# Kernel optimization log

Measured on AMD Instinct MI355X. Metric: run time of the kernel, lower is better.

Reference implementation:

```python
import jax, jax.numpy as jnp
import numpy as np

DIM = 1024
HEADS = 16
HEAD_DIM = DIM // HEADS
SCALE = HEAD_DIM ** -0.5


def setup_inputs() -> dict:
    key = jax.random.key(0)
    k1, k2, k3, k4 = jax.random.split(key, 4)
    x = jax.random.normal(k1, (8, 1024, DIM), dtype=jnp.float32)
    # qkv: Linear(dim, 3*dim), bias=False; proj: Linear(dim, dim) with bias
    w_qkv = jax.random.normal(k2, (DIM, 3 * DIM), dtype=jnp.float32) * (DIM ** -0.5)
    w_proj = jax.random.normal(k3, (DIM, DIM), dtype=jnp.float32) * (DIM ** -0.5)
    b_proj = jax.random.normal(k4, (DIM,), dtype=jnp.float32) * 0.02
    return {"x": x, "w_qkv": w_qkv, "w_proj": w_proj, "b_proj": b_proj}


def reference(x, w_qkv, w_proj, b_proj):
    b, n, dim = x.shape
    h, d = HEADS, HEAD_DIM
    qkv = x @ w_qkv                                  # [b, n, 3*dim]
    qkv = qkv.reshape(b, n, 3, h, d)                  # split (qkv h d)
    q = jnp.transpose(qkv[:, :, 0], (0, 2, 1, 3))     # [b, h, n, d]
    k = jnp.transpose(qkv[:, :, 1], (0, 2, 1, 3))
    v = jnp.transpose(qkv[:, :, 2], (0, 2, 1, 3))
    dots = jnp.einsum('bhid,bhjd->bhij', q, k) * SCALE
    attn = jax.nn.softmax(dots, axis=-1)              # [b, h, n, n]
    out = jnp.einsum('bhij,bhjd->bhid', attn, v)      # [b, h, n, d]
    out = jnp.transpose(out, (0, 2, 1, 3)).reshape(b, n, dim)
    return out @ w_proj + b_proj
```

## Files before the change

### kernel.cpp

```cpp
#include <hip/hip_runtime.h>
#include <hip/hip_bf16.h>
#include <stdint.h>


typedef __attribute__((ext_vector_type(8))) short  short8;
typedef __attribute__((ext_vector_type(4))) float  floatx4;

#define MFMA_BF16(a, b, c) __builtin_amdgcn_mfma_f32_16x16x32_bf16((a), (b), (c), 0, 0, 0)

__device__ __forceinline__ uint16_t f2b(float f) {
    uint32_t i; __builtin_memcpy(&i, &f, 4);
    uint32_t r = i + 0x7FFFu + ((i >> 16) & 1u);
    return (uint16_t)(r >> 16);
}

__device__ __forceinline__ uint32_t pk_bf16(float a, float b) {
    uint32_t u;
    asm("v_cvt_pk_bf16_f32 %0, %1, %2" : "=v"(u) : "v"(a), "v"(b));
    return u;
}

__device__ __forceinline__ float exp2_hw(float x) {
    float r; asm("v_exp_f32 %0, %1" : "=v"(r) : "v"(x)); return r;
}

__device__ __forceinline__ void p32swap(uint32_t& a, uint32_t& b) {
    asm("v_permlane32_swap_b32 %0, %1" : "+v"(a), "+v"(b));
}
__device__ __forceinline__ void p16swap(uint32_t& a, uint32_t& b) {
    asm("v_permlane16_swap_b32 %0, %1" : "+v"(a), "+v"(b));
}

__device__ __forceinline__ void async16(uint16_t* lds, const uint16_t* g) {
    __builtin_amdgcn_global_load_lds(
        (const __attribute__((address_space(1))) uint32_t*)g,
        (__attribute__((address_space(3))) uint32_t*)lds,
        16, 0, 0);
}

__global__ __launch_bounds__(256) void cvt_f32_bf16(
    const float* __restrict__ in, uint16_t* __restrict__ out, int n4)
{
    const int i = blockIdx.x * 256 + threadIdx.x;
    if (i < n4) {
        const float4 v = ((const float4*)in)[i];
        ushort4 o;
        o.x = f2b(v.x); o.y = f2b(v.y); o.z = f2b(v.z); o.w = f2b(v.w);
        ((ushort4*)out)[i] = o;
    }
}

__global__ __launch_bounds__(256) void transpose_k(
    const float* __restrict__ in, uint16_t* __restrict__ out, int R, int C)
{
    __shared__ uint16_t t[32][33];
    const int bx = blockIdx.x * 32;
    const int by = blockIdx.y * 32;
    const int tx = threadIdx.x & 31, ty = threadIdx.x >> 5;
    #pragma unroll
    for (int j = 0; j < 32; j += 8)
        t[ty + j][tx] = f2b(in[(size_t)(by + ty + j) * C + bx + tx]);
    __syncthreads();
    #pragma unroll
    for (int j = 0; j < 32; j += 8)
        out[(size_t)(bx + ty + j) * R + by + tx] = t[tx][ty + j];
}

template <int EPI>
__global__ __launch_bounds__(256, 2) void gemm_bt(
    const uint16_t* __restrict__ A, const uint16_t* __restrict__ Bt,
    uint16_t* __restrict__ C, float* __restrict__ Cf,
    const float* __restrict__ bias, int M, int N, int K)
{
    __shared__ uint16_t As[128 * 64];
    __shared__ uint16_t Bs[128 * 64];

    const int tid  = threadIdx.x;
    const int lane = tid & 63, quad = lane >> 4, l16 = lane & 15;
    const int wv   = tid >> 6;
    const int wm   = (wv >> 1) * 64, wn = (wv & 1) * 64;

    const int lid = blockIdx.y * gridDim.x + blockIdx.x;
    const int nxl = gridDim.x >> 3;
    const int xcd = lid & 7, loc = lid >> 3;
    const int bx  = xcd * nxl + (loc % nxl);
    const int by  = loc / nxl;
    const int tm  = by * 128, tn = bx * 128;

    floatx4 acc[4][4] = {};

    for (int kt = 0; kt < K; kt += 64) {
        __syncthreads();
        #pragma unroll
        for (int i = 0; i < 4; i++) {
            const int li  = i * 256 + tid;
            const int row = li >> 3;
            const int cg  = (li & 7) ^ (row & 7);
            async16(&As[li * 8], &A[(size_t)(tm + row) * K + kt + cg * 8]);
        }
        #pragma unroll
        for (int i = 0; i < 4; i++) {
            const int li  = i * 256 + tid;
            const int row = li >> 3;
            const int cg  = (li & 7) ^ (row & 7);
            async16(&Bs[li * 8], &Bt[(size_t)(tn + row) * K + kt + cg * 8]);
        }
        __syncthreads();
        #pragma unroll
        for (int kc = 0; kc < 2; kc++) {
            short8 af[4], bf[4];
            #pragma unroll
            for (int mb = 0; mb < 4; mb++) {
                const int row = wm + mb * 16 + l16;
                const int g   = kc * 4 + quad;
                af[mb] = *(const short8*)&As[row * 64 + ((g ^ (row & 7)) * 8)];
            }
            #pragma unroll
            for (int nb = 0; nb < 4; nb++) {
                const int row = wn + nb * 16 + l16;
                const int g   = kc * 4 + quad;
                bf[nb] = *(const short8*)&Bs[row * 64 + ((g ^ (row & 7)) * 8)];
            }
            #pragma unroll
            for (int mb = 0; mb < 4; mb++)
                #pragma unroll
                for (int nb = 0; nb < 4; nb++)
                    acc[mb][nb] = MFMA_BF16(af[mb], bf[nb], acc[mb][nb]);
        }
    }

    if (EPI == 0) {
        const int which = (tn + wn) >> 10;
        if (which == 2) {
            #pragma unroll
            for (int nb = 0; nb < 4; nb++) {
                const int col = tn + wn + nb * 16 + l16;
                const int hh = (col >> 6) & 15, dd = col & 63;
                #pragma unroll
                for (int mb = 0; mb < 4; mb++) {
                    const int gm = tm + wm + mb * 16 + quad * 4;
                    const int b  = gm >> 10, n = gm & 1023;
                    const size_t rgn = (size_t)(256 + b * 16 + hh) * 65536;
                    uint2 o;
                    o.x = pk_bf16(acc[mb][nb][0], acc[mb][nb][1]);
                    o.y = pk_bf16(acc[mb][nb][2], acc[mb][nb][3]);
                    *(uint2*)&C[rgn + (size_t)dd * 1024 + n] = o;
                }
            }
        } else {
            const float qs = (which == 0) ? 0.18033688011112043f : 1.0f;
            #pragma unroll
            for (int nb = 0; nb < 4; nb++) {
                const int col = tn + wn + nb * 16 + l16;
                const int hh = (col >> 6) & 15, dd = col & 63;
                #pragma unroll
                for (int mb = 0; mb < 4; mb++)
                    #pragma unroll
                    for (int r = 0; r < 4; r++) {
                        const int gm = tm + wm + mb * 16 + quad * 4 + r;
                        const int b  = gm >> 10, n = gm & 1023;
                        const size_t rgn = (size_t)(which * 128 + b * 16 + hh) * 65536;
                        C[rgn + (size_t)n * 64 + dd] = f2b(acc[mb][nb][r] * qs);
                    }
            }
        }
    } else {
        #pragma unroll
        for (int nb = 0; nb < 4; nb++) {
            const int col = tn + wn + nb * 16 + l16;
            const float bv = bias[col];
            #pragma unroll
            for (int mb = 0; mb < 4; mb++)
                #pragma unroll
                for (int r = 0; r < 4; r++) {
                    const int gm = tm + wm + mb * 16 + quad * 4 + r;
                    Cf[(size_t)gm * N + col] = acc[mb][nb][r] + bv;
                }
        }
    }
}

__global__ __launch_bounds__(256, 4) void attn_fa(
    const uint16_t* __restrict__ qkv, uint16_t* __restrict__ out)
{
    __shared__ uint16_t Ks[2][64 * 64];
    __shared__ uint16_t Vs[2][64 * 64];

    const int tid  = threadIdx.x;
    const int lane = tid & 63, quad = lane >> 4, l16 = lane & 15;
    const int wv   = tid >> 6;
    const int bh   = blockIdx.x;
    const int q0   = blockIdx.y * 128 + wv * 32;

    const size_t qbase  = (size_t)bh * 65536;
    const size_t kbase  = (size_t)(128 + bh) * 65536;
    const size_t vtbase = (size_t)(256 + bh) * 65536;

    short8 qf[2][2];
    #pragma unroll
    for (int nq = 0; nq < 2; nq++)
        #pragma unroll
        for (int ks = 0; ks < 2; ks++)
            qf[nq][ks] = *(const short8*)&qkv[qbase + (size_t)(q0 + nq * 16 + l16) * 64 + ks * 32 + quad * 8];
    asm volatile("s_waitcnt vmcnt(0)" ::: "memory");

    short8 ones;
    #pragma unroll
    for (int j = 0; j < 8; j++) ones[j] = (short)0x3F80;

    const int li0 = tid,        r0 = li0 >> 3, c0 = (li0 & 7) ^ (r0 & 7);
    const int li1 = 256 + tid,  r1 = li1 >> 3, c1 = (li1 & 7) ^ (r1 & 7);
    const uint16_t* kg0 = &qkv[kbase + (size_t)r0 * 64 + c0 * 8];
    const uint16_t* kg1 = &qkv[kbase + (size_t)r1 * 64 + c1 * 8];
    const uint16_t* vg0 = &qkv[vtbase + (size_t)r0 * 1024 + c0 * 8];
    const uint16_t* vg1 = &qkv[vtbase + (size_t)r1 * 1024 + c1 * 8];

    floatx4 Oacc[2][4] = {};
    floatx4 Lacc[2] = {};

    #pragma unroll
    for (int pb = 0; pb < 2; pb++) {
        async16(&Ks[pb][li0 * 8], kg0 + pb * 4096);
        async16(&Ks[pb][li1 * 8], kg1 + pb * 4096);
        async16(&Vs[pb][li0 * 8], vg0 + pb * 64);
        async16(&Vs[pb][li1 * 8], vg1 + pb * 64);
    }
    const uint16_t* sk0 = kg0 + 2 * 4096;
    const uint16_t* sk1 = kg1 + 2 * 4096;
    const uint16_t* sv0 = vg0 + 2 * 64;
    const uint16_t* sv1 = vg1 + 2 * 64;
    __builtin_amdgcn_sched_barrier(0);
    asm volatile("s_waitcnt vmcnt(4)" ::: "memory");
    __builtin_amdgcn_s_barrier();

    for (int kb = 0; kb < 16; kb++) {
        const uint16_t* Kc = &Ks[kb & 1][0];
        const uint16_t* Vc = &Vs[kb & 1][0];

        short8 pf[2][2];
        #pragma unroll
        for (int kk = 0; kk < 2; kk++) {
            floatx4 st[2][2];
            __builtin_amdgcn_s_setprio(1);
            #pragma unroll
            for (int mb2 = 0; mb2 < 2; mb2++) {
                const int krow = (kk * 2 + mb2) * 16 + l16;
                short8 kf0 = *(const short8*)&Kc[krow * 64 + ((quad ^ (krow & 7)) * 8)];
                short8 kf1 = *(const short8*)&Kc[krow * 64 + (((4 + quad) ^ (krow & 7)) * 8)];
                #pragma unroll
                for (int nq = 0; nq < 2; nq++) {
                    floatx4 z = {};
                    z = MFMA_BF16(kf0, qf[nq][0], z);
                    z = MFMA_BF16(kf1, qf[nq][1], z);
                    st[mb2][nq] = z;
                }
            }
            __builtin_amdgcn_s_setprio(0);
            #pragma unroll
            for (int nq = 0; nq < 2; nq++) {
                uint32_t w0 = pk_bf16(exp2_hw(st[0][nq][0]), exp2_hw(st[0][nq][1]));
                uint32_t w1 = pk_bf16(exp2_hw(st[0][nq][2]), exp2_hw(st[0][nq][3]));
                uint32_t w2 = pk_bf16(exp2_hw(st[1][nq][0]), exp2_hw(st[1][nq][1]));
                uint32_t w3 = pk_bf16(exp2_hw(st[1][nq][2]), exp2_hw(st[1][nq][3]));
                p32swap(w0, w2); p16swap(w0, w2);
                p32swap(w1, w3); p16swap(w1, w3);
                uint32_t w[4] = { w0, w1, w2, w3 };
                __builtin_memcpy(&pf[nq][kk], w, 16);
            }
            #pragma unroll
            for (int qb = 0; qb < 2; qb++)
                Lacc[qb] = MFMA_BF16(pf[qb][kk], ones, Lacc[qb]);
        }
        __builtin_amdgcn_s_setprio(1);
        #pragma unroll
        for (int nb = 0; nb < 4; nb++)
            #pragma unroll
            for (int kk = 0; kk < 2; kk++) {
                const int vrow = nb * 16 + l16;
                const int g    = kk * 4 + quad;
                short8 vf = *(const short8*)&Vc[vrow * 64 + ((g ^ (vrow & 7)) * 8)];
                #pragma unroll
                for (int qb = 0; qb < 2; qb++)
                    Oacc[qb][nb] = MFMA_BF16(pf[qb][kk], vf, Oacc[qb][nb]);
            }
        __builtin_amdgcn_s_setprio(0);

        __builtin_amdgcn_sched_barrier(0);
        __builtin_amdgcn_s_barrier();
        if (kb + 2 < 16) {
            uint16_t* Kd = &Ks[kb & 1][0];
            uint16_t* Vd = &Vs[kb & 1][0];
            async16(&Kd[li0 * 8], sk0);  sk0 += 4096;
            async16(&Kd[li1 * 8], sk1);  sk1 += 4096;
            async16(&Vd[li0 * 8], sv0);  sv0 += 64;
            async16(&Vd[li1 * 8], sv1);  sv1 += 64;
            __builtin_amdgcn_sched_barrier(0);
            asm volatile("s_waitcnt vmcnt(4)" ::: "memory");
        } else {
            __builtin_amdgcn_sched_barrier(0);
            asm volatile("s_waitcnt vmcnt(0)" ::: "memory");
        }
        __builtin_amdgcn_s_barrier();
        __builtin_amdgcn_sched_barrier(0);
    }

    float inv[2][4];
    #pragma unroll
    for (int qb = 0; qb < 2; qb++)
        #pragma unroll
        for (int r = 0; r < 4; r++)
            inv[qb][r] = 1.f / Lacc[qb][r];

    const int b = bh >> 4, hh = bh & 15;
    #pragma unroll
    for (int qb = 0; qb < 2; qb++)
        #pragma unroll
        for (int nb = 0; nb < 4; nb++)
            #pragma unroll
            for (int r = 0; r < 4; r++) {
                const int n = q0 + qb * 16 + quad * 4 + r;
                out[((size_t)(b * 1024 + n)) * 1024 + hh * 64 + nb * 16 + l16] =
                    f2b(Oacc[qb][nb][r] * inv[qb][r]);
            }
}

extern "C" void kernel_launch(void* const* d_in, const int* in_sizes, int n_in,
                              void* d_out, int out_size, void* d_ws, size_t ws_size,
                              hipStream_t stream)
{
    const float* x      = (const float*)d_in[0];
    const float* w_qkv  = (const float*)d_in[1];
    const float* w_proj = (const float*)d_in[2];
    const float* b_proj = (const float*)d_in[3];
    float* out = (float*)d_out;

    uint16_t* ws   = (uint16_t*)d_ws;
    uint16_t* xb   = ws;
    uint16_t* wTq  = xb  + 8192 * 1024;
    uint16_t* wTp  = wTq + 3072 * 1024;
    uint16_t* qkvb = wTp + 1024 * 1024;
    uint16_t* ao   = xb;

    cvt_f32_bf16<<<8192, 256, 0, stream>>>(x, xb, 8192 * 1024 / 4);
    transpose_k<<<dim3(96, 32), 256, 0, stream>>>(w_qkv, wTq, 1024, 3072);
    transpose_k<<<dim3(32, 32), 256, 0, stream>>>(w_proj, wTp, 1024, 1024);
    gemm_bt<0><<<dim3(24, 64), 256, 0, stream>>>(xb, wTq, qkvb, nullptr, nullptr, 8192, 3072, 1024);
    attn_fa<<<dim3(128, 8), 256, 0, stream>>>(qkvb, ao);
    gemm_bt<1><<<dim3(8, 64), 256, 0, stream>>>(ao, wTp, nullptr, out, b_proj, 8192, 1024, 1024);
}
```

Measured before the change: 222.0 us.

## Rewrite QKV GEMM with 256x256 tiles, 8 waves and interleaved async prefetch

Splits the templated GEMM into a dedicated QKV kernel and a projection kernel. The QKV kernel uses 512 threads, 256x256 output tiles and double-buffered LDS, with async loads for the next two k-steps spread across four sub-phases. It also adds explicit waitcnt and barrier scheduling, raises wave priority around the MFMA blocks, and remaps workgroups per XCD. The aim is to hide global-load latency and raise MFMA utilisation. The cost is 128KB of LDS per block, higher register pressure from 32 accumulators per lane, and fragile hand-tuned wait counts.

```diff
diff --git a/kernel.cpp b/kernel.cpp
--- a/kernel.cpp
+++ b/kernel.cpp
@@ -66,11 +66,155 @@
         out[(size_t)(bx + ty + j) * R + by + tx] = t[tx][ty + j];
 }
 
-template <int EPI>
-__global__ __launch_bounds__(256, 2) void gemm_bt(
+__global__ __launch_bounds__(512, 2) void gemm_qkv(
     const uint16_t* __restrict__ A, const uint16_t* __restrict__ Bt,
-    uint16_t* __restrict__ C, float* __restrict__ Cf,
-    const float* __restrict__ bias, int M, int N, int K)
+    uint16_t* __restrict__ C, int M, int N, int K)
+{
+    __shared__ uint16_t As[2][256 * 64];
+    __shared__ uint16_t Bs[2][256 * 64];
+
+    const int tid  = threadIdx.x;
+    const int lane = tid & 63, quad = lane >> 4, l16 = lane & 15;
+    const int wv   = tid >> 6;
+    const int wm   = (wv >> 2) * 128;
+    const int wn   = (wv & 3) * 64;
+
+    const int lid = blockIdx.y * gridDim.x + blockIdx.x;
+    const int cpx = (gridDim.x * gridDim.y) >> 3;
+    const int wgid = (lid & 7) * cpx + (lid >> 3);
+    const int bx  = wgid % gridDim.x;
+    const int by  = wgid / gridDim.x;
+    const int tm  = by * 256, tn = bx * 256;
+
+    const int nt = K >> 6;
+
+    const int sr  = tid >> 3;
+    const int sc  = tid & 7;
+    #define A_ROW(c) (((sr) < 32 ? (c) * 32 + (sr) : 128 + (c) * 32 + ((sr) - 32)))
+    #define B_ROW(j) ((j) * 64 + (sr))
+
+    #define STAGE_A(buf, kt, c)                                                   \
+        do { const int r_ = A_ROW(c); const int cg_ = sc ^ (r_ & 7);              \
+             async16(&As[buf][(r_ * 8 + sc) * 8],                                 \
+                     &A[(size_t)(tm + r_) * K + (kt) + cg_ * 8]); } while (0)
+    #define STAGE_B(buf, kt, j)                                                   \
+        do { const int r_ = B_ROW(j); const int cg_ = sc ^ (r_ & 7);              \
+             async16(&Bs[buf][(r_ * 8 + sc) * 8],                                 \
+                     &Bt[(size_t)(tn + r_) * K + (kt) + cg_ * 8]); } while (0)
+
+    floatx4 acc[8][4] = {};
+
+    STAGE_A(0, 0, 0); STAGE_A(0, 0, 1); STAGE_A(0, 0, 2); STAGE_A(0, 0, 3);
+    STAGE_B(0, 0, 0); STAGE_B(0, 0, 1); STAGE_B(0, 0, 2); STAGE_B(0, 0, 3);
+    STAGE_B(1, 64, 0); STAGE_B(1, 64, 1); STAGE_B(1, 64, 2); STAGE_B(1, 64, 3);
+    STAGE_A(1, 64, 0); STAGE_A(1, 64, 1); STAGE_A(1, 64, 2);
+    __builtin_amdgcn_sched_barrier(0);
+    asm volatile("s_waitcnt vmcnt(7)" ::: "memory");
+    __builtin_amdgcn_s_barrier();
+
+    for (int t = 0; t < nt; t++) {
+        const int cur = t & 1;
+        const uint16_t* Ac = &As[cur][0];
+        const uint16_t* Bc = &Bs[cur][0];
+        short8 bf[4][2];
+        #pragma unroll
+        for (int p = 0; p < 4; p++) {
+            short8 af[2][2];
+            #pragma unroll
+            for (int mb = 0; mb < 2; mb++) {
+                const int row = wm + p * 32 + mb * 16 + l16;
+                #pragma unroll
+                for (int kc = 0; kc < 2; kc++) {
+                    const int g = kc * 4 + quad;
+                    af[mb][kc] = *(const short8*)&Ac[row * 64 + ((g ^ (row & 7)) * 8)];
+                }
+            }
+            if (p == 0) {
+                #pragma unroll
+                for (int nb = 0; nb < 4; nb++) {
+                    const int row = wn + nb * 16 + l16;
+                    #pragma unroll
+                    for (int kc = 0; kc < 2; kc++) {
+                        const int g = kc * 4 + quad;
+                        bf[nb][kc] = *(const short8*)&Bc[row * 64 + ((g ^ (row & 7)) * 8)];
+                    }
+                }
+            }
+            if (p == 0) {
+                if (t + 1 < nt) STAGE_A(cur ^ 1, (t + 1) << 6, 3);
+            } else if (t + 2 < nt) {
+                const int kt2 = (t + 2) << 6;
+                if (p == 1) { STAGE_B(cur, kt2, 0); STAGE_B(cur, kt2, 1); STAGE_A(cur, kt2, 0); }
+                if (p == 2) { STAGE_B(cur, kt2, 2); STAGE_B(cur, kt2, 3); STAGE_A(cur, kt2, 1); }
+                if (p == 3) { STAGE_A(cur, kt2, 2); }
+            }
+            __builtin_amdgcn_sched_barrier(0);
+            __builtin_amdgcn_s_barrier();
+            asm volatile("s_waitcnt lgkmcnt(0)" ::: "memory");
+            __builtin_amdgcn_sched_barrier(0);
+            __builtin_amdgcn_s_setprio(1);
+            #pragma unroll
+            for (int mb = 0; mb < 2; mb++)
+                #pragma unroll
+                for (int nb = 0; nb < 4; nb++)
+                    #pragma unroll
+                    for (int kc = 0; kc < 2; kc++)
+                        acc[p * 2 + mb][nb] =
+                            MFMA_BF16(af[mb][kc], bf[nb][kc], acc[p * 2 + mb][nb]);
+            __builtin_amdgcn_s_setprio(0);
+            __builtin_amdgcn_sched_barrier(0);
+            if (p == 3) {
+                if (t + 2 < nt)      { asm volatile("s_waitcnt vmcnt(7)" ::: "memory"); }
+                else if (t + 1 < nt) { asm volatile("s_waitcnt vmcnt(0)" ::: "memory"); }
+            }
+            __builtin_amdgcn_s_barrier();
+            __builtin_amdgcn_sched_barrier(0);
+        }
+    }
+    #undef STAGE_A
+    #undef STAGE_B
+    #undef A_ROW
+    #undef B_ROW
+
+    const int which = (tn + wn) >> 10;
+    if (which == 2) {
+        #pragma unroll
+        for (int nb = 0; nb < 4; nb++) {
+            const int col = tn + wn + nb * 16 + l16;
+            const int hh = (col >> 6) & 15, dd = col & 63;
+            #pragma unroll
+            for (int mb = 0; mb < 8; mb++) {
+                const int gm = tm + wm + mb * 16 + quad * 4;
+                const int b  = gm >> 10, n = gm & 1023;
+                const size_t rgn = (size_t)(256 + b * 16 + hh) * 65536;
+                uint2 o;
+                o.x = pk_bf16(acc[mb][nb][0], acc[mb][nb][1]);
+                o.y = pk_bf16(acc[mb][nb][2], acc[mb][nb][3]);
+                *(uint2*)&C[rgn + (size_t)dd * 1024 + n] = o;
+            }
+        }
+    } else {
+        const float qs = (which == 0) ? 0.18033688011112043f : 1.0f;
+        #pragma unroll
+        for (int nb = 0; nb < 4; nb++) {
+            const int col = tn + wn + nb * 16 + l16;
+            const int hh = (col >> 6) & 15, dd = col & 63;
+            #pragma unroll
+            for (int mb = 0; mb < 8; mb++)
+                #pragma unroll
+                for (int r = 0; r < 4; r++) {
+                    const int gm = tm + wm + mb * 16 + quad * 4 + r;
+                    const int b  = gm >> 10, n = gm & 1023;
+                    const size_t rgn = (size_t)(which * 128 + b * 16 + hh) * 65536;
+                    C[rgn + (size_t)n * 64 + dd] = f2b(acc[mb][nb][r] * qs);
+                }
+        }
+    }
+}
+
+__global__ __launch_bounds__(256, 2) void gemm_proj(
+    const uint16_t* __restrict__ A, const uint16_t* __restrict__ Bt,
+    float* __restrict__ Cf, const float* __restrict__ bias, int M, int N, int K)
 {
     __shared__ uint16_t As[128 * 64];
     __shared__ uint16_t Bs[128 * 64];
@@ -129,54 +273,17 @@
         }
     }
 
-    if (EPI == 0) {
-        const int which = (tn + wn) >> 10;
-        if (which == 2) {
-            #pragma unroll
-            for (int nb = 0; nb < 4; nb++) {
-                const int col = tn + wn + nb * 16 + l16;
-                const int hh = (col >> 6) & 15, dd = col & 63;
-                #pragma unroll
-                for (int mb = 0; mb < 4; mb++) {
-                    const int gm = tm + wm + mb * 16 + quad * 4;
-                    const int b  = gm >> 10, n = gm & 1023;
-                    const size_t rgn = (size_t)(256 + b * 16 + hh) * 65536;
-                    uint2 o;
-                    o.x = pk_bf16(acc[mb][nb][0], acc[mb][nb][1]);
-                    o.y = pk_bf16(acc[mb][nb][2], acc[mb][nb][3]);
-                    *(uint2*)&C[rgn + (size_t)dd * 1024 + n] = o;
-                }
-            }
-        } else {
-            const float qs = (which == 0) ? 0.18033688011112043f : 1.0f;
-            #pragma unroll
-            for (int nb = 0; nb < 4; nb++) {
-                const int col = tn + wn + nb * 16 + l16;
-                const int hh = (col >> 6) & 15, dd = col & 63;
-                #pragma unroll
-                for (int mb = 0; mb < 4; mb++)
-                    #pragma unroll
-                    for (int r = 0; r < 4; r++) {
-                        const int gm = tm + wm + mb * 16 + quad * 4 + r;
-                        const int b  = gm >> 10, n = gm & 1023;
-                        const size_t rgn = (size_t)(which * 128 + b * 16 + hh) * 65536;
-                        C[rgn + (size_t)n * 64 + dd] = f2b(acc[mb][nb][r] * qs);
-                    }
-            }
-        }
-    } else {
-        #pragma unroll
-        for (int nb = 0; nb < 4; nb++) {
-            const int col = tn + wn + nb * 16 + l16;
-            const float bv = bias[col];
-            #pragma unroll
-            for (int mb = 0; mb < 4; mb++)
-                #pragma unroll
-                for (int r = 0; r < 4; r++) {
-                    const int gm = tm + wm + mb * 16 + quad * 4 + r;
-                    Cf[(size_t)gm * N + col] = acc[mb][nb][r] + bv;
-                }
-        }
+    #pragma unroll
+    for (int nb = 0; nb < 4; nb++) {
+        const int col = tn + wn + nb * 16 + l16;
+        const float bv = bias[col];
+        #pragma unroll
+        for (int mb = 0; mb < 4; mb++)
+            #pragma unroll
+            for (int r = 0; r < 4; r++) {
+                const int gm = tm + wm + mb * 16 + quad * 4 + r;
+                Cf[(size_t)gm * N + col] = acc[mb][nb][r] + bv;
+            }
     }
 }
 
@@ -344,7 +451,7 @@
     cvt_f32_bf16<<<8192, 256, 0, stream>>>(x, xb, 8192 * 1024 / 4);
     transpose_k<<<dim3(96, 32), 256, 0, stream>>>(w_qkv, wTq, 1024, 3072);
     transpose_k<<<dim3(32, 32), 256, 0, stream>>>(w_proj, wTp, 1024, 1024);
-    gemm_bt<0><<<dim3(24, 64), 256, 0, stream>>>(xb, wTq, qkvb, nullptr, nullptr, 8192, 3072, 1024);
+    gemm_qkv<<<dim3(12, 32), 512, 0, stream>>>(xb, wTq, qkvb, 8192, 3072, 1024);
     attn_fa<<<dim3(128, 8), 256, 0, stream>>>(qkvb, ao);
-    gemm_bt<1><<<dim3(8, 64), 256, 0, stream>>>(ao, wTp, nullptr, out, b_proj, 8192, 1024, 1024);
-}
+    gemm_proj<<<dim3(8, 64), 256, 0, stream>>>(ao, wTp, out, b_proj, 8192, 1024, 1024);
+}
```

New measurement: 235.1 us. 5.9% more time.
